# Performance work log

Measured on AMD Instinct MI355X. Metric: run time of the kernel, lower is better.

## Reference

```python
import jax, jax.numpy as jnp
import numpy as np

N, L, D = 32768, 15, 256
VOCAB, SCORE_MAX = 27, 100


def setup_inputs() -> dict:
    key = jax.random.key(0)
    ks = jax.random.split(key, 16)
    inp = {
        'words': jax.random.randint(ks[0], (N, L), 0, VOCAB, dtype=jnp.int32),
        'rows': jax.random.randint(ks[1], (N,), 0, L, dtype=jnp.int32),
        'cols': jax.random.randint(ks[2], (N,), 0, L, dtype=jnp.int32),
        'dirs': jax.random.randint(ks[3], (N,), 0, 2, dtype=jnp.int32),
        'scores': jax.random.randint(ks[4], (N,), 0, 150, dtype=jnp.int32),
        'letter_emb': jax.random.normal(ks[5], (VOCAB, D), jnp.float32),
        'positional': jax.random.normal(ks[6], (L, D), jnp.float32),
        'Wq': jax.random.normal(ks[7], (D, D), jnp.float32) / np.sqrt(D),
        'bq': jax.random.normal(ks[8], (D,), jnp.float32) * 0.01,
        'Wk': jax.random.normal(ks[9], (D, D), jnp.float32) / np.sqrt(D),
        'bk': jax.random.normal(ks[10], (D,), jnp.float32) * 0.01,
        'Wv': jax.random.normal(ks[11], (D, D), jnp.float32) / np.sqrt(D),
        'bv': jax.random.normal(ks[12], (D,), jnp.float32) * 0.01,
        'row_emb': jax.random.normal(ks[13], (L, D), jnp.float32),
        'col_emb': jax.random.normal(ks[14], (L, D), jnp.float32),
        'dir_emb': jax.random.normal(ks[15], (2, D), jnp.float32),
        'score_emb': jax.random.normal(jax.random.fold_in(key, 99), (SCORE_MAX, D), jnp.float32),
    }
    return inp


def reference(words, rows, cols, dirs, scores, letter_emb, positional, Wq, bq, Wk, bk, Wv, bv, row_emb, col_emb, dir_emb, score_emb):
    # WordEncoder: letter embedding + positional, then single-head self-attention, sum over positions
    emb = letter_emb[words] + positional[None, :, :]            # [N, L, D]
    q = emb @ Wq.T + bq                                          # [N, L, D]
    k = emb @ Wk.T + bk
    v = emb @ Wv.T + bv
    att = jax.nn.softmax(jnp.einsum('nld,nmd->nlm', q, k), axis=-1)  # [N, L, L]
    word = jnp.einsum('nlm,nmd->nd', att, v)                     # (att @ v).sum(axis=1) -> [N, D]
    # VectorEncoder
    vector = row_emb[rows] + col_emb[cols] + dir_emb[dirs]       # [N, D]
    # score embedding (clamped to score_max - 1)
    score_v = score_emb[jnp.minimum(scores, SCORE_MAX - 1)]      # [N, D]
    # original computes word_enc(move.word) twice (word + ordered) -> 2 * word
    return 2.0 * word + vector + score_v
```

## Files before the change

### kernel.cpp

```cpp
#include <hip/hip_runtime.h>
#include <hip/hip_bf16.h>

#define NMOV 32768
#define LW 15
#define DIM 256
#define NVOC 27
#define NR 405
#define GSH 408
#define MPB 8

__device__ __forceinline__ float b2f(unsigned short u) {
    return __uint_as_float(((unsigned int)u) << 16);
}

__global__ __launch_bounds__(256) void qkv_tables(
    const float* __restrict__ le, const float* __restrict__ pos,
    const float* __restrict__ Wq, const float* __restrict__ bq,
    const float* __restrict__ Wk, const float* __restrict__ bk,
    const float* __restrict__ Wv, const float* __restrict__ bv,
    float* __restrict__ QT, float* __restrict__ KT,
    __hip_bfloat16* __restrict__ VT)
{
    const int b   = blockIdx.x;
    const int c   = b / 15;
    const int rem = b % 15;
    const int lg  = rem / 3;
    const int mat = rem % 3;
    const int d   = threadIdx.x;

    const float* W  = (mat == 0) ? Wq : (mat == 1) ? Wk : Wv;
    const float* bb = (mat == 0) ? bq : (mat == 1) ? bk : bv;

    __shared__ float e[3][DIM];
    const float lv = le[c * DIM + d];
    #pragma unroll
    for (int k = 0; k < 3; ++k)
        e[k][d] = lv + pos[(lg * 3 + k) * DIM + d];
    __syncthreads();

    float acc[3];
    const float bias = bb[d];
    #pragma unroll
    for (int k = 0; k < 3; ++k) acc[k] = bias;

    const float4* w4 = (const float4*)(W + d * DIM);
    #pragma unroll 8
    for (int j4 = 0; j4 < DIM / 4; ++j4) {
        float4 w = w4[j4];
        #pragma unroll
        for (int k = 0; k < 3; ++k) {
            float4 e4 = *(const float4*)&e[k][j4 * 4];
            acc[k] += e4.x * w.x + e4.y * w.y + e4.z * w.z + e4.w * w.w;
        }
    }
    #pragma unroll
    for (int k = 0; k < 3; ++k) {
        int r = c * LW + lg * 3 + k;
        if (mat == 0)      QT[r * DIM + d] = acc[k];
        else if (mat == 1) KT[r * DIM + d] = acc[k];
        else               VT[r * DIM + d] = __float2bfloat16(acc[k]);
    }
}

__global__ __launch_bounds__(256) void h_matrix(
    const float* __restrict__ QT, const float* __restrict__ KT,
    float2* __restrict__ H)
{
    __shared__ float Qi[16][68], Ki[16][68], Qj[16][68], Kj[16][68];

    int rem = blockIdx.x, bi = 0, cnt = 26;
    while (rem >= cnt) { rem -= cnt; ++bi; --cnt; }
    const int bj = bi + rem;
    const int i0 = bi * 16, j0 = bj * 16;
    const int t = threadIdx.x;
    const int ti = t >> 4, tj = t & 15;

    float acc_ij = 0.f, acc_ji = 0.f;

    for (int k0 = 0; k0 < DIM; k0 += 64) {
        #pragma unroll
        for (int s = 0; s < 4; ++s) {
            int slot = s * 256 + t;
            int tile = slot >> 8;
            int r    = (slot >> 4) & 15;
            int c4   = slot & 15;
            int grow = (tile < 2) ? (i0 + r) : (j0 + r);
            const float* src = (tile == 0 || tile == 2) ? QT : KT;
            float4 v = (grow < NR)
                ? *(const float4*)&src[grow * DIM + k0 + c4 * 4]
                : make_float4(0.f, 0.f, 0.f, 0.f);
            float* dst = (tile == 0) ? &Qi[r][c4 * 4]
                       : (tile == 1) ? &Ki[r][c4 * 4]
                       : (tile == 2) ? &Qj[r][c4 * 4] : &Kj[r][c4 * 4];
            *(float4*)dst = v;
        }
        __syncthreads();
        #pragma unroll 4
        for (int k = 0; k < 64; k += 4) {
            float4 qi = *(const float4*)&Qi[ti][k];
            float4 kj = *(const float4*)&Kj[tj][k];
            float4 qj = *(const float4*)&Qj[ti][k];
            float4 ki = *(const float4*)&Ki[tj][k];
            acc_ij += qi.x * kj.x + qi.y * kj.y + qi.z * kj.z + qi.w * kj.w;
            acc_ji += qj.x * ki.x + qj.y * ki.y + qj.z * ki.z + qj.w * ki.w;
        }
        __syncthreads();
    }

    Qi[ti][tj] = acc_ij;
    Ki[ti][tj] = acc_ji;
    __syncthreads();
    const float t_ij = Qi[tj][ti];
    const float t_ji = Ki[tj][ti];

    const int i1 = i0 + ti, j1 = j0 + tj;
    if (i1 < NR && j1 < NR) H[i1 * GSH + j1] = make_float2(acc_ij, t_ji);
    const int i2 = j0 + ti, j2 = i0 + tj;
    if (i2 < NR && j2 < NR) H[i2 * GSH + j2] = make_float2(acc_ji, t_ij);
}

__global__ __launch_bounds__(256) void moves_kernel(
    const int* __restrict__ words, const int* __restrict__ rowsI,
    const int* __restrict__ colsI, const int* __restrict__ dirsI,
    const int* __restrict__ scoresI,
    const float2* __restrict__ H, const __hip_bfloat16* __restrict__ VT,
    const float* __restrict__ row_emb, const float* __restrict__ col_emb,
    const float* __restrict__ dir_emb, const float* __restrict__ score_emb,
    float* __restrict__ out)
{
    __shared__ float S[MPB][LW][17];
    __shared__ int   rIdx[MPB * LW];
    __shared__ float csum[MPB][16];
    __shared__ int   meta[4][MPB];
    const int base = blockIdx.x * MPB;
    const int t = threadIdx.x;

    if (t < MPB * LW)
        rIdx[t] = words[base * LW + t] * LW + (t % LW);
    if (t < 4 * MPB) {
        int sel = t >> 3, j = t & 7;
        const int* src = (sel == 0) ? rowsI : (sel == 1) ? colsI
                       : (sel == 2) ? dirsI : scoresI;
        int v = src[base + j];
        meta[sel][j] = (sel == 3) ? min(v, 99) : v;
    }
    __syncthreads();

    const int mv = t >> 5, j = t & 31;
    #pragma unroll
    for (int k = 0; k < 4; ++k) {
        int p = j + 32 * k;
        if (p < 120) {
            int l = (int)((sqrtf(8.f * (float)p + 1.f) - 1.f) * 0.5f);
            if (l * (l + 1) / 2 > p) --l;
            int m = p - l * (l + 1) / 2;
            int rl = rIdx[mv * LW + l], rm = rIdx[mv * LW + m];
            float2 hv = H[rl * GSH + rm];
            S[mv][l][m] = hv.x;
            S[mv][m][l] = hv.y;
        }
    }
    __syncthreads();

    if (j < LW) {
        float s[LW];
        #pragma unroll
        for (int m = 0; m < LW; ++m) s[m] = S[mv][j][m];
        float mx = s[0];
        #pragma unroll
        for (int m = 1; m < LW; ++m) mx = fmaxf(mx, s[m]);
        float sum = 0.f;
        #pragma unroll
        for (int m = 0; m < LW; ++m) { s[m] = __expf(s[m] - mx); sum += s[m]; }
        float inv = 1.0f / sum;
        #pragma unroll
        for (int m = 0; m < LW; ++m) S[mv][j][m] = s[m] * inv;
    }
    __syncthreads();

    if (j < LW) {
        float acc = 0.f;
        #pragma unroll
        for (int l = 0; l < LW; ++l) acc += S[mv][l][j];
        csum[mv][j] = acc;
    }
    __syncthreads();

    const int wv = t >> 6;
    const int d0 = (t & 63) * 4;
    #pragma unroll
    for (int s2 = 0; s2 < 2; ++s2) {
        const int i = wv * 2 + s2;
        float wx = 0.f, wy = 0.f, wz = 0.f, ww = 0.f;
        #pragma unroll
        for (int m = 0; m < LW; ++m) {
            float c = csum[i][m];
            int r = rIdx[i * LW + m];
            ushort4 vv = *(const ushort4*)((const unsigned short*)VT + r * DIM + d0);
            wx += c * b2f(vv.x); wy += c * b2f(vv.y);
            wz += c * b2f(vv.z); ww += c * b2f(vv.w);
        }
        const int n = base + i;
        float4 re = *(const float4*)&row_emb[meta[0][i] * DIM + d0];
        float4 ce = *(const float4*)&col_emb[meta[1][i] * DIM + d0];
        float4 de = *(const float4*)&dir_emb[meta[2][i] * DIM + d0];
        float4 se = *(const float4*)&score_emb[meta[3][i] * DIM + d0];
        float4 res;
        res.x = 2.f * wx + re.x + ce.x + de.x + se.x;
        res.y = 2.f * wy + re.y + ce.y + de.y + se.y;
        res.z = 2.f * wz + re.z + ce.z + de.z + se.z;
        res.w = 2.f * ww + re.w + ce.w + de.w + se.w;
        *(float4*)&out[n * DIM + d0] = res;
    }
}

extern "C" void kernel_launch(void* const* d_in, const int* in_sizes, int n_in,
                              void* d_out, int out_size, void* d_ws, size_t ws_size,
                              hipStream_t stream)
{
    const int*   words      = (const int*)d_in[0];
    const int*   rowsI      = (const int*)d_in[1];
    const int*   colsI      = (const int*)d_in[2];
    const int*   dirsI      = (const int*)d_in[3];
    const int*   scoresI    = (const int*)d_in[4];
    const float* letter_emb = (const float*)d_in[5];
    const float* positional = (const float*)d_in[6];
    const float* Wq         = (const float*)d_in[7];
    const float* bq         = (const float*)d_in[8];
    const float* Wk         = (const float*)d_in[9];
    const float* bk         = (const float*)d_in[10];
    const float* Wv         = (const float*)d_in[11];
    const float* bv         = (const float*)d_in[12];
    const float* row_emb    = (const float*)d_in[13];
    const float* col_emb    = (const float*)d_in[14];
    const float* dir_emb    = (const float*)d_in[15];
    const float* score_emb  = (const float*)d_in[16];
    float* out = (float*)d_out;

    float*  QT = (float*)d_ws;
    float*  KT = QT + NR * DIM;
    float2* Hm = (float2*)(KT + NR * DIM);
    __hip_bfloat16* VT = (__hip_bfloat16*)((char*)Hm + (size_t)NR * GSH * sizeof(float2));

    qkv_tables<<<405, 256, 0, stream>>>(letter_emb, positional, Wq, bq, Wk, bk,
                                        Wv, bv, QT, KT, VT);
    h_matrix<<<351, 256, 0, stream>>>(QT, KT, Hm);
    moves_kernel<<<NMOV / MPB, 256, 0, stream>>>(words, rowsI, colsI, dirsI,
                                                 scoresI, Hm, VT, row_emb,
                                                 col_emb, dir_emb, score_emb,
                                                 out);
}
```

Baseline: 67.49 us.

## Make moves kernel wave-local: drop block barriers, LUT pair indices, direct meta loads

Each 64-lane wavefront already owns two moves end to end, so the four block-wide __syncthreads are replaced with wave barriers and the per-wave word indices are loaded by that wave itself. The sqrt-based triangular index decode is replaced by a 120-entry byte lookup table. The shared staging of the row, col, dir and score indices is removed in favour of direct global loads in the output phase, and the launch bounds now request higher occupancy. The aim is to cut block-level synchronisation stalls and ALU work. The correctness of the wave barriers depends on the wave64 mapping on this GPU.

```diff
diff --git a/kernel.cpp b/kernel.cpp
--- a/kernel.cpp
+++ b/kernel.cpp
@@ -12,6 +12,24 @@
 __device__ __forceinline__ float b2f(unsigned short u) {
     return __uint_as_float(((unsigned int)u) << 16);
 }
+
+__device__ const unsigned char PAIR_LUT[120] = {
+    0x00,
+    0x10,0x11,
+    0x20,0x21,0x22,
+    0x30,0x31,0x32,0x33,
+    0x40,0x41,0x42,0x43,0x44,
+    0x50,0x51,0x52,0x53,0x54,0x55,
+    0x60,0x61,0x62,0x63,0x64,0x65,0x66,
+    0x70,0x71,0x72,0x73,0x74,0x75,0x76,0x77,
+    0x80,0x81,0x82,0x83,0x84,0x85,0x86,0x87,0x88,
+    0x90,0x91,0x92,0x93,0x94,0x95,0x96,0x97,0x98,0x99,
+    0xA0,0xA1,0xA2,0xA3,0xA4,0xA5,0xA6,0xA7,0xA8,0xA9,0xAA,
+    0xB0,0xB1,0xB2,0xB3,0xB4,0xB5,0xB6,0xB7,0xB8,0xB9,0xBA,0xBB,
+    0xC0,0xC1,0xC2,0xC3,0xC4,0xC5,0xC6,0xC7,0xC8,0xC9,0xCA,0xCB,0xCC,
+    0xD0,0xD1,0xD2,0xD3,0xD4,0xD5,0xD6,0xD7,0xD8,0xD9,0xDA,0xDB,0xDC,0xDD,
+    0xE0,0xE1,0xE2,0xE3,0xE4,0xE5,0xE6,0xE7,0xE8,0xE9,0xEA,0xEB,0xEC,0xED,0xEE
+};
 
 __global__ __launch_bounds__(256) void qkv_tables(
     const float* __restrict__ le, const float* __restrict__ pos,
@@ -119,7 +137,7 @@
     if (i2 < NR && j2 < NR) H[i2 * GSH + j2] = make_float2(acc_ji, t_ij);
 }
 
-__global__ __launch_bounds__(256) void moves_kernel(
+__global__ __launch_bounds__(256, 8) void moves_kernel(
     const int* __restrict__ words, const int* __restrict__ rowsI,
     const int* __restrict__ colsI, const int* __restrict__ dirsI,
     const int* __restrict__ scoresI,
@@ -129,38 +147,30 @@
     float* __restrict__ out)
 {
     __shared__ float S[MPB][LW][17];
-    __shared__ int   rIdx[MPB * LW];
+    __shared__ int   rIdx[MPB][16];
     __shared__ float csum[MPB][16];
-    __shared__ int   meta[4][MPB];
     const int base = blockIdx.x * MPB;
     const int t = threadIdx.x;
-
-    if (t < MPB * LW)
-        rIdx[t] = words[base * LW + t] * LW + (t % LW);
-    if (t < 4 * MPB) {
-        int sel = t >> 3, j = t & 7;
-        const int* src = (sel == 0) ? rowsI : (sel == 1) ? colsI
-                       : (sel == 2) ? dirsI : scoresI;
-        int v = src[base + j];
-        meta[sel][j] = (sel == 3) ? min(v, 99) : v;
-    }
-    __syncthreads();
-
-    const int mv = t >> 5, j = t & 31;
+    const int mv = t >> 5;
+    const int j  = t & 31;
+
+    if (j < LW)
+        rIdx[mv][j] = words[(base + mv) * LW + j] * LW + j;
+    __builtin_amdgcn_wave_barrier();
+
     #pragma unroll
     for (int k = 0; k < 4; ++k) {
         int p = j + 32 * k;
         if (p < 120) {
-            int l = (int)((sqrtf(8.f * (float)p + 1.f) - 1.f) * 0.5f);
-            if (l * (l + 1) / 2 > p) --l;
-            int m = p - l * (l + 1) / 2;
-            int rl = rIdx[mv * LW + l], rm = rIdx[mv * LW + m];
-            float2 hv = H[rl * GSH + rm];
+            int lm = PAIR_LUT[p];
+            int l = lm >> 4, m = lm & 15;
+            int rl = rIdx[mv][l], rm = rIdx[mv][m];
+            float2 hv = H[(size_t)rl * GSH + rm];
             S[mv][l][m] = hv.x;
             S[mv][m][l] = hv.y;
         }
     }
-    __syncthreads();
+    __builtin_amdgcn_wave_barrier();
 
     if (j < LW) {
         float s[LW];
@@ -176,7 +186,7 @@
         #pragma unroll
         for (int m = 0; m < LW; ++m) S[mv][j][m] = s[m] * inv;
     }
-    __syncthreads();
+    __builtin_amdgcn_wave_barrier();
 
     if (j < LW) {
         float acc = 0.f;
@@ -184,33 +194,33 @@
         for (int l = 0; l < LW; ++l) acc += S[mv][l][j];
         csum[mv][j] = acc;
     }
-    __syncthreads();
+    __builtin_amdgcn_wave_barrier();
 
     const int wv = t >> 6;
     const int d0 = (t & 63) * 4;
     #pragma unroll
     for (int s2 = 0; s2 < 2; ++s2) {
         const int i = wv * 2 + s2;
+        const int n = base + i;
         float wx = 0.f, wy = 0.f, wz = 0.f, ww = 0.f;
         #pragma unroll
         for (int m = 0; m < LW; ++m) {
             float c = csum[i][m];
-            int r = rIdx[i * LW + m];
-            ushort4 vv = *(const ushort4*)((const unsigned short*)VT + r * DIM + d0);
+            int r = rIdx[i][m];
+            ushort4 vv = *(const ushort4*)((const unsigned short*)VT + (size_t)r * DIM + d0);
             wx += c * b2f(vv.x); wy += c * b2f(vv.y);
             wz += c * b2f(vv.z); ww += c * b2f(vv.w);
         }
-        const int n = base + i;
-        float4 re = *(const float4*)&row_emb[meta[0][i] * DIM + d0];
-        float4 ce = *(const float4*)&col_emb[meta[1][i] * DIM + d0];
-        float4 de = *(const float4*)&dir_emb[meta[2][i] * DIM + d0];
-        float4 se = *(const float4*)&score_emb[meta[3][i] * DIM + d0];
+        float4 re = *(const float4*)&row_emb[rowsI[n] * DIM + d0];
+        float4 ce = *(const float4*)&col_emb[colsI[n] * DIM + d0];
+        float4 de = *(const float4*)&dir_emb[dirsI[n] * DIM + d0];
+        float4 se = *(const float4*)&score_emb[min(scoresI[n], 99) * DIM + d0];
         float4 res;
         res.x = 2.f * wx + re.x + ce.x + de.x + se.x;
         res.y = 2.f * wy + re.y + ce.y + de.y + se.y;
         res.z = 2.f * wz + re.z + ce.z + de.z + se.z;
         res.w = 2.f * ww + re.w + ce.w + de.w + se.w;
-        *(float4*)&out[n * DIM + d0] = res;
+        *(float4*)&out[(size_t)n * DIM + d0] = res;
     }
 }
 
```

New measurement: 77.24 us. 14.5% more time.
